# Kernel tuning notes

Hardware: AMD Instinct MI355X
Metric: run time of the kernel (lower is better)

Reference implementation:

```python
import jax, jax.numpy as jnp
import numpy as np
from jax import lax

B, C, H, W = 4, 256, 64, 64
O = 256
EPS = 1e-5


def setup_inputs() -> dict:
    key = jax.random.key(0)
    ks = jax.random.split(key, 20)
    s = 0.02
    d = {
        'input1': jax.random.normal(ks[0], (B, C, H, W), jnp.float32),
        'input2': jax.random.normal(ks[1], (B, C, H, W), jnp.float32),
        'wq1': jax.random.normal(ks[2], (C // 8, C), jnp.float32) * s,
        'bq1': jnp.zeros((C // 8,), jnp.float32),
        'wk1': jax.random.normal(ks[3], (C // 4, C), jnp.float32) * s,
        'bk1': jnp.zeros((C // 4,), jnp.float32),
        'wv1': jax.random.normal(ks[4], (C, C), jnp.float32) * s,
        'bv1': jnp.zeros((C,), jnp.float32),
        'wq2': jax.random.normal(ks[5], (C // 8, C), jnp.float32) * s,
        'bq2': jnp.zeros((C // 8,), jnp.float32),
        'wk2': jax.random.normal(ks[6], (C // 4, C), jnp.float32) * s,
        'bk2': jnp.zeros((C // 4,), jnp.float32),
        'wv2': jax.random.normal(ks[7], (C, C), jnp.float32) * s,
        'bv2': jnp.zeros((C,), jnp.float32),
        'gamma': jnp.asarray([0.1], jnp.float32),
        'w_cat': jax.random.normal(ks[8], (O, 2 * C, 3, 3), jnp.float32) * s,
        'bn_scale': jnp.ones((O,), jnp.float32),
        'bn_bias': jnp.zeros((O,), jnp.float32),
        'bn_mean': jnp.zeros((O,), jnp.float32),
        'bn_var': jnp.ones((O,), jnp.float32),
    }
    return d


def _conv1x1(x, w, b):
    # x: [B,C,H,W], w: [Co,C] -> [B,Co,H,W]
    return jnp.einsum('bchw,oc->bohw', x, w) + b[None, :, None, None]


def reference(input1, input2, wq1, bq1, wk1, bk1, wv1, bv1,
              wq2, bq2, wk2, bk2, wv2, bv2, gamma, w_cat,
              bn_scale, bn_bias, bn_mean, bn_var):
    b, c, h, w = input1.shape
    hw = h * w
    q1 = _conv1x1(input1, wq1, bq1)
    k1 = _conv1x1(input1, wk1, bk1).reshape(b, -1, hw)
    v1 = _conv1x1(input1, wv1, bv1).reshape(b, -1, hw)
    q2 = _conv1x1(input2, wq2, bq2)
    k2 = _conv1x1(input2, wk2, bk2).reshape(b, -1, hw)
    v2 = _conv1x1(input2, wv2, bv2).reshape(b, -1, hw)
    # concat q heads along channel -> [B, C/4, HW] -> [B, HW, C/4]
    q = jnp.concatenate([q1, q2], axis=1).reshape(b, -1, hw).transpose(0, 2, 1)
    # branch 1: [B,HW,HW] scores (no scaling, as in source)
    attn1 = jax.nn.softmax(jnp.einsum('bnc,bcm->bnm', q, k1), axis=-1)
    out1 = jnp.einsum('bcm,bnm->bcn', v1, attn1).reshape(b, c, h, w)
    out1 = gamma[0] * out1 + input1
    # branch 2
    attn2 = jax.nn.softmax(jnp.einsum('bnc,bcm->bnm', q, k2), axis=-1)
    out2 = jnp.einsum('bcm,bnm->bcn', v2, attn2).reshape(b, c, h, w)
    out2 = gamma[0] * out2 + input2
    # conv_cat: 3x3 conv (no bias) + BatchNorm (eval stats) + ReLU
    cat = jnp.concatenate([out1, out2], axis=1)
    conv = lax.conv_general_dilated(cat, w_cat, (1, 1), 'SAME',
                                    dimension_numbers=('NCHW', 'OIHW', 'NCHW'))
    inv = bn_scale / jnp.sqrt(bn_var + EPS)
    bn = conv * inv[None, :, None, None] + (bn_bias - bn_mean * inv)[None, :, None, None]
    feat_sum = jax.nn.relu(bn)
    return (feat_sum, out1, out2)
```

## Files before the change

kernel.cpp:

```cpp
#include <hip/hip_runtime.h>
#include <hip/hip_bf16.h>

#define HW 4096

#define KT_OFF   1048576
#define WTP_OFF  1572864
#define O1_OFF   4194304
#define WVB_OFF  1179648
#define XBF_OFF  1310720
#define WS_NEED  19398656ull
#define WS_NEED2 20463616ull

typedef short v8s  __attribute__((ext_vector_type(8)));
typedef float v16f __attribute__((ext_vector_type(16)));

#define LSTR 72
#define ZSTR 264
#define CPAD 20
#define PL_ROWS 128
#define PL_SZ  (2 * PL_ROWS * LSTR)
#define XP_SZ  (2 * 256 * LSTR)
#define XLHALF (4 * 66 * CPAD)
#define CPYCH  69696
#define CPYB   2230272

__device__ __forceinline__ unsigned short f2b(float f) {
    unsigned u = __float_as_uint(f);
    return (unsigned short)((u + 0x7fffu + ((u >> 16) & 1u)) >> 16);
}
__device__ __forceinline__ unsigned cvt_pk_bf16(float lo, float hi) {
    float2 f2; f2.x = lo; f2.y = hi;
    __hip_bfloat162 h = __float22bfloat162_rn(f2);
    unsigned r;
    __builtin_memcpy(&r, &h, 4);
    return r;
}
__device__ __forceinline__ v8s load8(const unsigned short* p) {
    union { uint2 u[2]; v8s v; } t;
    t.u[0] = *(const uint2*)p;
    t.u[1] = *(const uint2*)(p + 4);
    return t.v;
}

__global__ __launch_bounds__(256) void wprep_proj(
    const float* __restrict__ wq1, const float* __restrict__ wk1, const float* __restrict__ wv1,
    const float* __restrict__ wq2, const float* __restrict__ wk2, const float* __restrict__ wv2,
    float* __restrict__ wtp) {
    int idx = blockIdx.x * 256 + threadIdx.x;
    if (idx >= 2 * 256 * 352) return;
    int sel = idx / 90112;
    int r   = idx - sel * 90112;
    int c   = r / 352;
    int co  = r - c * 352;
    const float* w; int row;
    if (co < 32)      { w = sel ? wq2 : wq1; row = co; }
    else if (co < 96) { w = sel ? wk2 : wk1; row = co - 32; }
    else              { w = sel ? wv2 : wv1; row = co - 96; }
    wtp[idx] = w[row * 256 + c];
}

__global__ __launch_bounds__(256) void wprep_convw(const float* __restrict__ wcat,
                                                   unsigned short* __restrict__ wt) {
    int i = blockIdx.x * 256 + threadIdx.x;
    if (i >= 32 * 9 * 256 * 16) return;
    const int ci_l = i & 15;
    const int o    = (i >> 4) & 255;
    const int t2   = i >> 12;
    const int tap  = t2 % 9;
    const int chunk = t2 / 9;
    wt[i] = f2b(wcat[((size_t)o * 512 + chunk * 16 + ci_l) * 9 + tap]);
}

__global__ __launch_bounds__(256) void wprep_wv(const float* __restrict__ wv1,
                                                const float* __restrict__ wv2,
                                                unsigned short* __restrict__ out) {
    int i = blockIdx.x * 256 + threadIdx.x;
    if (i >= 131072) return;
    const float* src = (i < 65536) ? wv1 : wv2;
    out[i] = f2b(src[i & 65535]);
}

__global__ __launch_bounds__(256) void wprep_xbf(const float* __restrict__ x1,
                                                 const float* __restrict__ x2,
                                                 unsigned short* __restrict__ xbf) {
    const size_t e = ((size_t)blockIdx.x * 256 + threadIdx.x) * 8;
    if (e >= 8388608) return;
    const float* src = (e < 4194304) ? (x1 + e) : (x2 + (e - 4194304));
    const float4 a = *(const float4*)src;
    const float4 c = *(const float4*)(src + 4);
    uint4 o;
    o.x = cvt_pk_bf16(a.x, a.y); o.y = cvt_pk_bf16(a.z, a.w);
    o.z = cvt_pk_bf16(c.x, c.y); o.w = cvt_pk_bf16(c.z, c.w);
    *(uint4*)&xbf[e] = o;
}

__global__ __launch_bounds__(256) void proj_kernel(
    const float* __restrict__ x1, const float* __restrict__ x2,
    const float* __restrict__ bq1, const float* __restrict__ bk1,
    const float* __restrict__ bq2, const float* __restrict__ bk2,
    float* __restrict__ dout) {
    __shared__ __align__(16) float xls[256][64];
    const int tile = blockIdx.x, sel = blockIdx.y, b = blockIdx.z;
    const int n0 = tile * 64;
    const float* xb = (sel ? x2 : x1) + (size_t)b * 256 * HW;

    for (int i = threadIdx.x; i < 4096; i += 256) {
        const int row = i >> 4, c4 = (i & 15) * 4;
        *(float4*)&xls[row][c4] = *(const float4*)(xb + (size_t)row * HW + n0 + c4);
    }
    __syncthreads();

    const int n   = threadIdx.x & 63;
    const int cog = __builtin_amdgcn_readfirstlane(threadIdx.x >> 6);
    const float* bq = sel ? bq2 : bq1;
    const float* bk = sel ? bk2 : bk1;
    const float* wc = dout + WTP_OFF + (size_t)sel * 90112;
    unsigned short* qtg = (unsigned short*)dout + (size_t)b * HW * 64;
    unsigned short* ktg = (unsigned short*)dout + KT_OFF + (size_t)(sel * 4 + b) * HW * 64;

    for (int blk = 0; blk < 3; ++blk) {
        const int co0 = cog * 24 + blk * 8;
        float acc[8];
        const float* brow; int r0; bool isq;
        if (co0 < 32) { r0 = co0;      brow = bq; isq = true;  }
        else          { r0 = co0 - 32; brow = bk; isq = false; }
        #pragma unroll
        for (int k = 0; k < 8; ++k) acc[k] = brow[r0 + k];
        #pragma unroll 4
        for (int c = 0; c < 256; ++c) {
            const float xv = xls[c][n];
            const float4 w0 = *(const float4*)(wc + (size_t)c * 352 + co0);
            const float4 w1 = *(const float4*)(wc + (size_t)c * 352 + co0 + 4);
            acc[0] += xv * w0.x; acc[1] += xv * w0.y; acc[2] += xv * w0.z; acc[3] += xv * w0.w;
            acc[4] += xv * w1.x; acc[5] += xv * w1.y; acc[6] += xv * w1.z; acc[7] += xv * w1.w;
        }
        unsigned pk2[4];
        #pragma unroll
        for (int k = 0; k < 4; ++k) pk2[k] = cvt_pk_bf16(acc[2 * k], acc[2 * k + 1]);
        unsigned short* dst = isq ? (qtg + (size_t)(n0 + n) * 64 + sel * 32 + r0)
                                  : (ktg + (size_t)(n0 + n) * 64 + r0);
        *(uint4*)dst = *(const uint4*)pk2;
    }
}

template <int USEBF>
__global__ __launch_bounds__(512, 2) void attn_kernel(
    const float* __restrict__ in1, const float* __restrict__ in2,
    const unsigned short* __restrict__ xbf,
    const unsigned short* __restrict__ wvbf,
    const float* __restrict__ bv1, const float* __restrict__ bv2,
    const float* __restrict__ gamma_p,
    float* __restrict__ dout) {
    __shared__ __align__(16) unsigned short smem[PL_SZ + XP_SZ];
    __shared__ float rsums[128][2];
    __shared__ float lfin[128];

    const int bid = blockIdx.x;
    const int g   = bid & 7;
    const int qt  = bid >> 3;
    const int br  = g >> 2, b = g & 3;
    const int t = threadIdx.x;
    const int w = t >> 6, lane = t & 63, h = lane >> 5, l32 = lane & 31;

    const unsigned short* qtg = (const unsigned short*)dout + (size_t)b * HW * 64;
    const unsigned short* ktg = (const unsigned short*)dout + KT_OFF + (size_t)(br * 4 + b) * HW * 64;
    const float* xg = (br ? in2 : in1) + (size_t)b * 256 * HW;
    float* zo = dout + O1_OFF + (size_t)br * 4194304 + (size_t)b * 256 * HW;

    const int msub = (w & 1) * 32;
    const int nsub = (w >> 1) * 32;
    const int cs   = w & 3;
    const int nh   = w >> 2;
    const int koff = h * 8;

    unsigned short* plds = smem;
    unsigned short* xp   = smem + PL_SZ;

    v8s aq[4];
    #pragma unroll
    for (int ks = 0; ks < 4; ++ks)
        aq[ks] = *(const v8s*)(qtg + (size_t)(qt * 128 + nsub + l32) * 64 + ks * 16 + koff);

    const unsigned short* kpt = ktg + (size_t)(msub + l32) * 64 + koff;
    v8s kf[4];
    #pragma unroll
    for (int ks = 0; ks < 4; ++ks)
        kf[ks] = *(const v8s*)(kpt + ks * 16);

    const int m4 = (t & 15) * 4, r0i = t >> 4;
    const float* xgp = xg + (size_t)r0i * HW + m4;
    const unsigned short* xbp = xbf + (size_t)br * 4194304
                              + (size_t)b * 256 * HW + (size_t)r0i * HW + m4;

    uint2 xpk[8];
    if constexpr (USEBF) {
        #pragma unroll
        for (int j = 0; j < 8; ++j) xpk[j] = *(const uint2*)(xbp + (size_t)j * 32 * HW);
    } else {
        float4 xr0[8];
        #pragma unroll
        for (int j = 0; j < 8; ++j) xr0[j] = *(const float4*)(xgp + (size_t)j * 32 * HW);
        #pragma unroll
        for (int j = 0; j < 8; ++j) {
            xpk[j].x = cvt_pk_bf16(xr0[j].x, xr0[j].y);
            xpk[j].y = cvt_pk_bf16(xr0[j].z, xr0[j].w);
        }
    }

    v16f a00, a01, a10, a11;
    #pragma unroll
    for (int i = 0; i < 16; ++i) { a00[i] = 0.f; a01[i] = 0.f; a10[i] = 0.f; a11[i] = 0.f; }
    float racc = 0.f;

    #pragma unroll 1
    for (int mt = 0; mt < 64; ++mt) {
        const int cur = mt & 1;
        v16f s;
        #pragma unroll
        for (int i = 0; i < 16; ++i) s[i] = 0.f;
        #pragma unroll
        for (int ks = 0; ks < 4; ++ks)
            s = __builtin_amdgcn_mfma_f32_32x32x16_bf16(kf[ks], aq[ks], s, 0, 0, 0);
        const int mg = (mt < 63) ? (mt + 1) * 64 : 0;
        #pragma unroll
        for (int ks = 0; ks < 4; ++ks)
            kf[ks] = *(const v8s*)(kpt + (size_t)mg * 64 + ks * 16);
        float4 xr[8];
        if constexpr (!USEBF) {
            #pragma unroll
            for (int j = 0; j < 8; ++j)
                xr[j] = *(const float4*)(xgp + (size_t)j * 32 * HW + mg);
        }
        unsigned short* prow = plds + (size_t)(cur * PL_ROWS + nsub + l32) * LSTR + msub;
        #pragma unroll
        for (int rp = 0; rp < 8; ++rp) {
            const float e0 = __expf(s[2 * rp]);
            const float e1 = __expf(s[2 * rp + 1]);
            racc += e0 + e1;
            const int m0 = ((2 * rp) & 3) + 8 * (rp >> 1) + 4 * h;
            *(unsigned*)&prow[m0] = cvt_pk_bf16(e0, e1);
        }
        {
            unsigned short* xw = xp + (size_t)(cur * 256 + r0i) * LSTR + m4;
            #pragma unroll
            for (int j = 0; j < 8; ++j)
                *(uint2*)(xw + (size_t)j * 32 * LSTR) = xpk[j];
        }
        if constexpr (USEBF) {
            #pragma unroll
            for (int j = 0; j < 8; ++j)
                xpk[j] = *(const uint2*)(xbp + (size_t)j * 32 * HW + mg);
        }
        __syncthreads();
        {
            const unsigned short* xb0 = xp + (size_t)(cur * 256 + cs * 64 + l32) * LSTR;
            const unsigned short* xb1 = xb0 + (size_t)32 * LSTR;
            const unsigned short* pb0 = plds + (size_t)(cur * PL_ROWS + nh * 64 + l32) * LSTR;
            const unsigned short* pb1 = pb0 + (size_t)32 * LSTR;
            #pragma unroll
            for (int ks = 0; ks < 4; ++ks) {
                const int mo = ks * 16 + koff;
                const v8s xa0 = *(const v8s*)(xb0 + mo);
                const v8s xa1 = *(const v8s*)(xb1 + mo);
                const v8s pf0 = *(const v8s*)(pb0 + mo);
                const v8s pf1 = *(const v8s*)(pb1 + mo);
                a00 = __builtin_amdgcn_mfma_f32_32x32x16_bf16(xa0, pf0, a00, 0, 0, 0);
                a01 = __builtin_amdgcn_mfma_f32_32x32x16_bf16(xa0, pf1, a01, 0, 0, 0);
                a10 = __builtin_amdgcn_mfma_f32_32x32x16_bf16(xa1, pf0, a10, 0, 0, 0);
                a11 = __builtin_amdgcn_mfma_f32_32x32x16_bf16(xa1, pf1, a11, 0, 0, 0);
            }
        }
        if constexpr (!USEBF) {
            #pragma unroll
            for (int j = 0; j < 8; ++j) {
                xpk[j].x = cvt_pk_bf16(xr[j].x, xr[j].y);
                xpk[j].y = cvt_pk_bf16(xr[j].z, xr[j].w);
            }
        }
    }
    __syncthreads();
    {
        const float rtot = racc + __shfl_xor(racc, 32);
        if (lane < 32) rsums[nsub + l32][w & 1] = rtot;
    }
    __syncthreads();
    if (t < 128) lfin[t] = 1.0f / (rsums[t][0] + rsums[t][1]);
    __syncthreads();
    const float dn0 = lfin[nh * 64 + l32];
    const float dn1 = lfin[nh * 64 + 32 + l32];
    unsigned short (*zt)[ZSTR] = (unsigned short (*)[ZSTR])smem;
    #pragma unroll
    for (int rp = 0; rp < 8; ++rp) {
        const int r = rp * 2;
        const int c = cs * 64 + (r & 3) + 8 * (r >> 2) + 4 * h;
        const int n0r = nh * 64 + l32, n1r = nh * 64 + 32 + l32;
        *(unsigned*)&zt[n0r][c]      = cvt_pk_bf16(a00[r] * dn0, a00[r + 1] * dn0);
        *(unsigned*)&zt[n1r][c]      = cvt_pk_bf16(a01[r] * dn1, a01[r + 1] * dn1);
        *(unsigned*)&zt[n0r][c + 32] = cvt_pk_bf16(a10[r] * dn0, a10[r + 1] * dn0);
        *(unsigned*)&zt[n1r][c + 32] = cvt_pk_bf16(a11[r] * dn1, a11[r + 1] * dn1);
    }
    __syncthreads();
    const unsigned short* wvb = wvbf + (size_t)br * 65536;
    const float* bvp = br ? bv2 : bv1;
    const float gamma = gamma_p[0];
    const int ob = cs * 64;
    const int ncol = qt * 128 + nh * 64;
    v16f m00, m01, m10, m11;
    #pragma unroll
    for (int i = 0; i < 16; ++i) { m00[i] = 0.f; m01[i] = 0.f; m10[i] = 0.f; m11[i] = 0.f; }
    #pragma unroll
    for (int ks = 0; ks < 16; ++ks) {
        const int k = ks * 16 + koff;
        const v8s aA = *(const v8s*)(wvb + (size_t)(ob + l32) * 256 + k);
        const v8s aB = *(const v8s*)(wvb + (size_t)(ob + 32 + l32) * 256 + k);
        const v8s b0v = *(const v8s*)&zt[nh * 64 + l32][k];
        const v8s b1v = *(const v8s*)&zt[nh * 64 + 32 + l32][k];
        m00 = __builtin_amdgcn_mfma_f32_32x32x16_bf16(aA, b0v, m00, 0, 0, 0);
        m01 = __builtin_amdgcn_mfma_f32_32x32x16_bf16(aA, b1v, m01, 0, 0, 0);
        m10 = __builtin_amdgcn_mfma_f32_32x32x16_bf16(aB, b0v, m10, 0, 0, 0);
        m11 = __builtin_amdgcn_mfma_f32_32x32x16_bf16(aB, b1v, m11, 0, 0, 0);
    }
    #pragma unroll
    for (int r = 0; r < 16; ++r) {
        const int o = ob + (r & 3) + 8 * (r >> 2) + 4 * h;
        const float bvA = bvp[o], bvB = bvp[o + 32];
        const size_t base0 = (size_t)o * HW + ncol;
        const size_t base1 = (size_t)(o + 32) * HW + ncol;
        zo[base0 + l32]      = gamma * (m00[r] + bvA) + xg[base0 + l32];
        zo[base0 + 32 + l32] = gamma * (m01[r] + bvA) + xg[base0 + 32 + l32];
        zo[base1 + l32]      = gamma * (m10[r] + bvB) + xg[base1 + l32];
        zo[base1 + 32 + l32] = gamma * (m11[r] + bvB) + xg[base1 + 32 + l32];
    }
}

__global__ __launch_bounds__(256) void cpy_pad(const float* __restrict__ dsrc,
                                               unsigned short* __restrict__ cpy) {
    __shared__ float xls[16][65];
    const int hp = blockIdx.x, chunk = blockIdx.y, b = blockIdx.z;
    const int t = threadIdx.x;
    unsigned short* crow = cpy + (((size_t)(b * 32 + chunk) * 66 + hp) * 66) * 16;
    if (hp == 0 || hp == 65) {
        if (t < 132) *(uint4*)(crow + t * 8) = make_uint4(0, 0, 0, 0);
        return;
    }
    const int hh = hp - 1;
    const float* src = dsrc + O1_OFF + (size_t)(chunk < 16 ? 0 : 1) * 4194304
                     + (size_t)b * 1048576 + (size_t)((chunk & 15) * 16) * HW + (size_t)hh * 64;
    {
        const int ci = t >> 6, ww = t & 63;
        #pragma unroll
        for (int j = 0; j < 4; ++j)
            xls[ci + 4 * j][ww] = src[(size_t)(ci + 4 * j) * HW + ww];
    }
    __syncthreads();
    {
        const int wwp = t >> 2, q = t & 3;
        uint2 pk;
        pk.x = cvt_pk_bf16(xls[q * 4 + 0][wwp], xls[q * 4 + 1][wwp]);
        pk.y = cvt_pk_bf16(xls[q * 4 + 2][wwp], xls[q * 4 + 3][wwp]);
        *(uint2*)(crow + (size_t)(wwp + 1) * 16 + q * 4) = pk;
    }
    if (t < 4) {
        unsigned short* p = crow + (size_t)(t >> 1) * 65 * 16 + (t & 1) * 8;
        *(uint4*)p = make_uint4(0, 0, 0, 0);
    }
}

__global__ __launch_bounds__(256, 4) void conv_bf(
    const unsigned short* __restrict__ wt,
    const unsigned short* __restrict__ cpy,
    const float* __restrict__ bn_scale, const float* __restrict__ bn_bias,
    const float* __restrict__ bn_mean,  const float* __restrict__ bn_var,
    float* __restrict__ dout) {
    const int bid = blockIdx.x;
    const int lin = (bid & 7) * 128 + (bid >> 3);
    const int ot  = lin & 7;
    const int g   = lin >> 3;
    const int pt  = g & 31, b = g >> 5;
    const int h0  = pt * 2;
    const int t   = threadIdx.x;
    const int w   = t >> 6, lane = t & 63, h = lane >> 5, l32 = lane & 31;
    const int n   = w * 32 + l32;
    const int r0  = n >> 6, c0 = n & 63;

    const unsigned short* wb = wt + (size_t)(ot * 32 + l32) * 16 + h * 8;
    const unsigned short* cb = cpy + (size_t)b * CPYB
                             + (size_t)(h0 + r0) * 66 * 16 + (size_t)c0 * 16 + h * 8;

    v16f acc;
    #pragma unroll
    for (int i = 0; i < 16; ++i) acc[i] = 0.f;

    #pragma unroll 1
    for (int chunk = 0; chunk < 32; ++chunk) {
        const unsigned short* wc = wb + (size_t)chunk * 9 * 4096;
        const unsigned short* cc = cb + (size_t)chunk * CPYCH;
        v8s wf[9], xf[9];
        #pragma unroll
        for (int tap = 0; tap < 9; ++tap) {
            const int dy = tap / 3, dx = tap % 3;
            wf[tap] = *(const v8s*)(wc + (size_t)tap * 4096);
            xf[tap] = *(const v8s*)(cc + (size_t)(dy * 66 + dx) * 16);
        }
        #pragma unroll
        for (int tap = 0; tap < 9; ++tap)
            acc = __builtin_amdgcn_mfma_f32_32x32x16_bf16(wf[tap], xf[tap], acc, 0, 0, 0);
    }
    const size_t gp = (size_t)(h0 + r0) * 64 + c0;
    #pragma unroll
    for (int r = 0; r < 16; ++r) {
        const int o_g = ot * 32 + (r & 3) + 8 * (r >> 2) + 4 * h;
        const float iv = bn_scale[o_g] * __frsqrt_rn(bn_var[o_g] + 1e-5f);
        const float ad = bn_bias[o_g] - bn_mean[o_g] * iv;
        float v = acc[r] * iv + ad;
        v = v > 0.f ? v : 0.f;
        dout[((size_t)b * 256 + o_g) * HW + gp] = v;
    }
}

__global__ __launch_bounds__(256) void conv_kernel(
    const unsigned short* __restrict__ wt,
    const float* __restrict__ bn_scale, const float* __restrict__ bn_bias,
    const float* __restrict__ bn_mean,  const float* __restrict__ bn_var,
    float* __restrict__ dout) {
    __shared__ __align__(16) unsigned short xl[2][4][66][CPAD];
    __shared__ __align__(16) unsigned short wl[2][9][64][CPAD];

    const int bid = blockIdx.x;
    const int xcd = bid & 7, j = bid >> 3;
    const int G   = xcd * 16 + (j >> 2);
    const int ot  = j & 3;
    const int pt  = G & 31;
    const int b   = G >> 5;
    const int h0 = pt * 2;
    const int t  = threadIdx.x;
    const int w  = t >> 6, lane = t & 63, h = lane >> 5, l32 = lane & 31;
    const int osub = (w & 1) * 32;
    const int ps0  = (w >> 1) * 64;

    int ldsoff[9], srcoff[9]; bool valid[9], inb[9];
    #pragma unroll
    for (int k = 0; k < 9; ++k) {
        const int i = t + k * 256;
        valid[k] = i < 2112;
        const int col = i % 66, rem = i / 66;
        const int row = rem & 3, cp = rem >> 2;
        const int hh = h0 + row - 1, ww = col - 1;
        inb[k] = (hh >= 0 && hh < 64 && ww >= 0 && ww < 64);
        srcoff[k] = 2 * cp * HW + (inb[k] ? hh * 64 + ww : 0);
        ldsoff[k] = (row * 66 + col) * CPAD + 2 * cp;
    }
    unsigned short* xlf = &xl[0][0][0][0];

    float inv[16], add[16];
    #pragma unroll
    for (int r = 0; r < 16; ++r) {
        const int o_g = ot * 64 + osub + (r & 3) + 8 * (r >> 2) + 4 * h;
        const float iv = bn_scale[o_g] * __frsqrt_rn(bn_var[o_g] + 1e-5f);
        inv[r] = iv;
        add[r] = bn_bias[o_g] - bn_mean[o_g] * iv;
    }

    v16f acc0, acc1;
    #pragma unroll
    for (int i = 0; i < 16; ++i) { acc0[i] = 0.f; acc1[i] = 0.f; }

    const float* bsrc = dout + O1_OFF + (size_t)b * 1048576;
    const unsigned short* wbase = wt + (size_t)(ot * 64) * 16;

    float xv0[9], xv1[9];
    uint2 wr[9];
    {
        const float* src = bsrc;
        #pragma unroll
        for (int k = 0; k < 9; ++k) {
            xv0[k] = 0.f; xv1[k] = 0.f;
            if (valid[k] && inb[k]) {
                const float* p = src + srcoff[k];
                xv0[k] = p[0]; xv1[k] = p[HW];
            }
        }
        #pragma unroll
        for (int u9 = 0; u9 < 9; ++u9) {
            const int u = t + u9 * 256;
            const int tap = u >> 8, rem2 = u & 255;
            const int o = rem2 >> 2, q = rem2 & 3;
            wr[u9] = *(const uint2*)(wbase + ((size_t)tap * 256 + o) * 16 + q * 4);
        }
    }

    #pragma unroll 1
    for (int chunk = 0; chunk < 32; ++chunk) {
        const int cur = chunk & 1;
        #pragma unroll
        for (int k = 0; k < 9; ++k)
            if (valid[k])
                *(unsigned*)&xlf[cur * XLHALF + ldsoff[k]] = cvt_pk_bf16(xv0[k], xv1[k]);
        #pragma unroll
        for (int u9 = 0; u9 < 9; ++u9) {
            const int u = t + u9 * 256;
            const int tap = u >> 8, rem2 = u & 255;
            const int o = rem2 >> 2, q = rem2 & 3;
            *(uint2*)&wl[cur][tap][o][q * 4] = wr[u9];
        }
        if (chunk < 31) {
            const int cn = chunk + 1;
            const float* src = bsrc + (size_t)(cn < 16 ? 0 : 1) * 4194304
                             + (size_t)((cn & 15) * 16) * HW;
            #pragma unroll
            for (int k = 0; k < 9; ++k) {
                xv0[k] = 0.f; xv1[k] = 0.f;
                if (valid[k] && inb[k]) {
                    const float* p = src + srcoff[k];
                    xv0[k] = p[0]; xv1[k] = p[HW];
                }
            }
            const unsigned short* wsl = wbase + (size_t)cn * 36864;
            #pragma unroll
            for (int u9 = 0; u9 < 9; ++u9) {
                const int u = t + u9 * 256;
                const int tap = u >> 8, rem2 = u & 255;
                const int o = rem2 >> 2, q = rem2 & 3;
                wr[u9] = *(const uint2*)(wsl + ((size_t)tap * 256 + o) * 16 + q * 4);
            }
        }
        __syncthreads();
        #pragma unroll
        for (int dy = 0; dy < 3; ++dy) {
            #pragma unroll
            for (int dx = 0; dx < 3; ++dx) {
                const v8s af = load8(&wl[cur][dy * 3 + dx][osub + l32][h * 8]);
                const int n0 = ps0 + l32, n1 = ps0 + 32 + l32;
                const v8s b0 = load8(&xl[cur][(n0 >> 6) + dy][(n0 & 63) + dx][h * 8]);
                const v8s b1 = load8(&xl[cur][(n1 >> 6) + dy][(n1 & 63) + dx][h * 8]);
                acc0 = __builtin_amdgcn_mfma_f32_32x32x16_bf16(af, b0, acc0, 0, 0, 0);
                acc1 = __builtin_amdgcn_mfma_f32_32x32x16_bf16(af, b1, acc1, 0, 0, 0);
            }
        }
    }
    const int px0 = ps0 + l32, px1 = ps0 + 32 + l32;
    const size_t gpx0 = (size_t)(h0 + (px0 >> 6)) * 64 + (px0 & 63);
    const size_t gpx1 = (size_t)(h0 + (px1 >> 6)) * 64 + (px1 & 63);
    #pragma unroll
    for (int r = 0; r < 16; ++r) {
        const int o_g = ot * 64 + osub + (r & 3) + 8 * (r >> 2) + 4 * h;
        const size_t obase = ((size_t)b * 256 + o_g) * HW;
        float v0 = acc0[r] * inv[r] + add[r];
        float v1 = acc1[r] * inv[r] + add[r];
        v0 = v0 > 0.f ? v0 : 0.f;
        v1 = v1 > 0.f ? v1 : 0.f;
        dout[obase + gpx0] = v0;
        dout[obase + gpx1] = v1;
    }
}

extern "C" void kernel_launch(void* const* d_in, const int* in_sizes, int n_in,
                              void* d_out, int out_size, void* d_ws, size_t ws_size,
                              hipStream_t stream) {
    (void)in_sizes; (void)n_in; (void)out_size;
    const float* x1   = (const float*)d_in[0];
    const float* x2   = (const float*)d_in[1];
    const float* wq1  = (const float*)d_in[2];
    const float* bq1  = (const float*)d_in[3];
    const float* wk1  = (const float*)d_in[4];
    const float* bk1  = (const float*)d_in[5];
    const float* wv1  = (const float*)d_in[6];
    const float* bv1  = (const float*)d_in[7];
    const float* wq2  = (const float*)d_in[8];
    const float* bq2  = (const float*)d_in[9];
    const float* wk2  = (const float*)d_in[10];
    const float* bk2  = (const float*)d_in[11];
    const float* wv2  = (const float*)d_in[12];
    const float* bv2  = (const float*)d_in[13];
    const float* gma  = (const float*)d_in[14];
    const float* wcat = (const float*)d_in[15];
    const float* bns  = (const float*)d_in[16];
    const float* bnb  = (const float*)d_in[17];
    const float* bnm  = (const float*)d_in[18];
    const float* bnv  = (const float*)d_in[19];

    float* out = (float*)d_out;
    unsigned short* wtc = (unsigned short*)d_ws;
    unsigned short* wvb = wtc + WVB_OFF;
    unsigned short* xbf = wtc + XBF_OFF;
    const bool use_bf  = ws_size >= WS_NEED;
    const bool use_cvb = ws_size >= WS_NEED2;

    wprep_proj<<<704, 256, 0, stream>>>(wq1, wk1, wv1, wq2, wk2, wv2, out + WTP_OFF);
    wprep_convw<<<4608, 256, 0, stream>>>(wcat, wtc);
    wprep_wv<<<512, 256, 0, stream>>>(wv1, wv2, wvb);
    if (use_bf) wprep_xbf<<<4096, 256, 0, stream>>>(x1, x2, xbf);
    proj_kernel<<<dim3(64, 2, 4), 256, 0, stream>>>(x1, x2, bq1, bk1, bq2, bk2, out);
    if (use_bf)
        attn_kernel<1><<<256, 512, 0, stream>>>(x1, x2, xbf, wvb, bv1, bv2, gma, out);
    else
        attn_kernel<0><<<256, 512, 0, stream>>>(x1, x2, xbf, wvb, bv1, bv2, gma, out);
    if (use_cvb) {
        cpy_pad<<<dim3(66, 32, 4), 256, 0, stream>>>(out, xbf);
        conv_bf<<<1024, 256, 0, stream>>>(wtc, xbf, bns, bnb, bnm, bnv, out);
    } else {
        conv_kernel<<<512, 256, 0, stream>>>(wtc, bns, bnb, bnm, bnv, out);
    }
}
```

Measured before the change: 424.3 us.

## Stage conv input halo tile in LDS with register prefetch double buffer

The 3x3 conv kernel now loads each chunk's padded 4-row by 66-column input tile into shared memory once and reads all nine taps from there, instead of issuing nine separate global loads per tap. The next chunk's tile is prefetched into registers while the current chunk is computed, and the shared tile is double-buffered. This is meant to cut redundant global and L2 traffic for the overlapping tap windows. In exchange it adds a block barrier per chunk and uses LDS, which could limit occupancy.

```diff
diff --git a/kernel.cpp b/kernel.cpp
--- a/kernel.cpp
+++ b/kernel.cpp
@@ -23,6 +23,7 @@
 #define XLHALF (4 * 66 * CPAD)
 #define CPYCH  69696
 #define CPYB   2230272
+#define V5SL   4224
 
 __device__ __forceinline__ unsigned short f2b(float f) {
     unsigned u = __float_as_uint(f);
@@ -366,12 +367,14 @@
     }
 }
 
-__global__ __launch_bounds__(256, 4) void conv_bf(
+__global__ __launch_bounds__(256, 4) void conv_v5(
     const unsigned short* __restrict__ wt,
     const unsigned short* __restrict__ cpy,
     const float* __restrict__ bn_scale, const float* __restrict__ bn_bias,
     const float* __restrict__ bn_mean,  const float* __restrict__ bn_var,
     float* __restrict__ dout) {
+    __shared__ __align__(16) unsigned short xl[2][V5SL];
+
     const int bid = blockIdx.x;
     const int lin = (bid & 7) * 128 + (bid >> 3);
     const int ot  = lin & 7;
@@ -380,31 +383,52 @@
     const int h0  = pt * 2;
     const int t   = threadIdx.x;
     const int w   = t >> 6, lane = t & 63, h = lane >> 5, l32 = lane & 31;
-    const int n   = w * 32 + l32;
-    const int r0  = n >> 6, c0 = n & 63;
-
+    const int px  = w * 32 + l32;
+    const int r0  = px >> 6, c0 = px & 63;
+
+    const unsigned short* cb = cpy + (size_t)b * CPYB + (size_t)h0 * 66 * 16;
     const unsigned short* wb = wt + (size_t)(ot * 32 + l32) * 16 + h * 8;
-    const unsigned short* cb = cpy + (size_t)b * CPYB
-                             + (size_t)(h0 + r0) * 66 * 16 + (size_t)c0 * 16 + h * 8;
 
     v16f acc;
     #pragma unroll
     for (int i = 0; i < 16; ++i) acc[i] = 0.f;
+
+    uint4 xs[3]; bool xv[3];
+    #pragma unroll
+    for (int j = 0; j < 3; ++j) {
+        const int idx = j * 256 + t;
+        xv[j] = idx < 528;
+        if (xv[j]) xs[j] = *(const uint4*)(cb + (size_t)idx * 8);
+    }
 
     #pragma unroll 1
     for (int chunk = 0; chunk < 32; ++chunk) {
-        const unsigned short* wc = wb + (size_t)chunk * 9 * 4096;
-        const unsigned short* cc = cb + (size_t)chunk * CPYCH;
-        v8s wf[9], xf[9];
-        #pragma unroll
-        for (int tap = 0; tap < 9; ++tap) {
-            const int dy = tap / 3, dx = tap % 3;
-            wf[tap] = *(const v8s*)(wc + (size_t)tap * 4096);
-            xf[tap] = *(const v8s*)(cc + (size_t)(dy * 66 + dx) * 16);
-        }
-        #pragma unroll
-        for (int tap = 0; tap < 9; ++tap)
-            acc = __builtin_amdgcn_mfma_f32_32x32x16_bf16(wf[tap], xf[tap], acc, 0, 0, 0);
+        const int cur = chunk & 1;
+        #pragma unroll
+        for (int j = 0; j < 3; ++j)
+            if (xv[j]) *(uint4*)&xl[cur][(size_t)(j * 256 + t) * 8] = xs[j];
+        v8s wf[9];
+        {
+            const unsigned short* wc = wb + (size_t)chunk * 36864;
+            #pragma unroll
+            for (int tap = 0; tap < 9; ++tap)
+                wf[tap] = *(const v8s*)(wc + (size_t)tap * 4096);
+        }
+        if (chunk < 31) {
+            const unsigned short* cn = cb + (size_t)(chunk + 1) * CPYCH;
+            #pragma unroll
+            for (int j = 0; j < 3; ++j)
+                if (xv[j]) xs[j] = *(const uint4*)(cn + (size_t)(j * 256 + t) * 8);
+        }
+        __syncthreads();
+        #pragma unroll
+        for (int dy = 0; dy < 3; ++dy) {
+            #pragma unroll
+            for (int dx = 0; dx < 3; ++dx) {
+                const v8s bf = *(const v8s*)&xl[cur][(size_t)((r0 + dy) * 66 + c0 + dx) * 16 + h * 8];
+                acc = __builtin_amdgcn_mfma_f32_32x32x16_bf16(wf[dy * 3 + dx], bf, acc, 0, 0, 0);
+            }
+        }
     }
     const size_t gp = (size_t)(h0 + r0) * 64 + c0;
     #pragma unroll
@@ -597,7 +621,7 @@
         attn_kernel<0><<<256, 512, 0, stream>>>(x1, x2, xbf, wvb, bv1, bv2, gma, out);
     if (use_cvb) {
         cpy_pad<<<dim3(66, 32, 4), 256, 0, stream>>>(out, xbf);
-        conv_bf<<<1024, 256, 0, stream>>>(wtc, xbf, bns, bnb, bnm, bnv, out);
+        conv_v5<<<1024, 256, 0, stream>>>(wtc, xbf, bns, bnb, bnm, bnv, out);
     } else {
         conv_kernel<<<512, 256, 0, stream>>>(wtc, bns, bnb, bnm, bnv, out);
     }
```

After: 465.5 us. 1.1x slower.
